# Performance work log

Hardware: AMD Instinct MI355X
Metric: run time of the kernel (lower is better)

Reference implementation:

```python
import jax, jax.numpy as jnp
import numpy as np

B, MAXR = 2048, 512
REQ_IN, REQ_HID, EMB1, EMB2 = 64, 256, 256, 128
INST_IN, CONCAT_HID = 64, 512


def setup_inputs() -> dict:
    key = jax.random.key(0)
    ks = jax.random.split(key, 10)
    inp = {
        "x_inst": jax.random.normal(ks[0], (B, INST_IN), dtype=jnp.float32),
        "x_req": jax.random.normal(ks[1], (B, MAXR, REQ_IN), dtype=jnp.float32),
        "x_n_req": jax.random.randint(ks[2], (B,), 0, MAXR, dtype=jnp.int32),
        # weights stored [in, out]; torch Linear has no bias for the req MLP
        "W_in": jax.random.normal(ks[3], (REQ_IN, REQ_HID), dtype=jnp.float32) / np.sqrt(REQ_IN),
        "W_e1": jax.random.normal(ks[4], (REQ_HID, EMB1), dtype=jnp.float32) / np.sqrt(REQ_HID),
        "W_e2": jax.random.normal(ks[5], (EMB1, EMB2), dtype=jnp.float32) / np.sqrt(EMB1),
        "W_c": jax.random.normal(ks[6], (INST_IN + EMB2, CONCAT_HID), dtype=jnp.float32) / np.sqrt(INST_IN + EMB2),
        "b_c": jax.random.normal(ks[7], (CONCAT_HID,), dtype=jnp.float32) * 0.01,
        "W_o": jax.random.normal(ks[8], (CONCAT_HID, 1), dtype=jnp.float32) / np.sqrt(CONCAT_HID),
        "b_o": jax.random.normal(ks[9], (1,), dtype=jnp.float32) * 0.01,
    }
    return inp


def reference(x_inst, x_req, x_n_req, W_in, W_e1, W_e2, W_c, b_c, W_o, b_o):
    act = jax.nn.relu
    # per-request MLP: [B, MAXR, REQ_IN] -> [B, MAXR, EMB1]
    h = act(jnp.einsum('bri,ih->brh', x_req, W_in))
    h = act(jnp.einsum('brh,he->bre', h, W_e1))
    # mask out padded requests (ragged lengths), then sum-pool over requests
    mask = (jnp.arange(MAXR)[None, :] < x_n_req[:, None])  # [B, MAXR]
    pooled = jnp.einsum('bre,br->be', h, mask.astype(h.dtype))  # [B, EMB1]
    req_embed = act(pooled @ W_e2)  # [B, EMB2]
    x = jnp.concatenate([x_inst, req_embed], axis=1)
    x = act(x @ W_c + b_c)
    return x @ W_o + b_o  # [B, 1]
```

## Files before the change

kernel.cpp:

```cpp
#include <hip/hip_runtime.h>


typedef __bf16 bf16x8 __attribute__((ext_vector_type(8)));
typedef __bf16 bf16x4 __attribute__((ext_vector_type(4)));
typedef float f32x4 __attribute__((ext_vector_type(4)));

#define MFMA16(a, b, c) __builtin_amdgcn_mfma_f32_16x16x32_bf16((a), (b), (c), 0, 0, 0)

#define G_BLOCKS 512

#define ASYNC_COPY16_NT(gsrc, ldst)                                   \
  __builtin_amdgcn_global_load_lds(                                   \
      (__attribute__((address_space(1))) void*)(gsrc),                \
      (__attribute__((address_space(3))) void*)(ldst), 16, 0, 2)

__global__ __launch_bounds__(256) void prep(const float* __restrict__ Win,
                                            const float* __restrict__ We1,
                                            const int* __restrict__ n_req,
                                            __bf16* __restrict__ WinT,
                                            __bf16* __restrict__ We1T,
                                            unsigned int* __restrict__ worklist,
                                            int* __restrict__ wl_count,
                                            float* __restrict__ zbuf) {
  if (blockIdx.x < 320) {
    int t = blockIdx.x * 256 + threadIdx.x;
    if (t < 16384) {
      int nn = t >> 6, k = t & 63;
      WinT[t] = (__bf16)Win[k * 256 + nn];
    } else {
      int e = t - 16384;
      int nn = e >> 8, k = e & 255;
      We1T[e] = (__bf16)We1[k * 256 + nn];
    }
    return;
  }
  ((float4*)zbuf)[threadIdx.x] = make_float4(0.f, 0.f, 0.f, 0.f);
  __shared__ int wsum[4];
  const int tid = threadIdx.x;
  const int base = tid * 8;
  int nt[8], s = 0;
#pragma unroll
  for (int j = 0; j < 8; ++j) {
    int n = n_req[base + j];
    nt[j] = (n + 63) >> 6;
    s += nt[j];
  }
  const int lane = tid & 63, wv = tid >> 6;
  int inc = s;
#pragma unroll
  for (int d = 1; d < 64; d <<= 1) {
    int u = __shfl_up(inc, d);
    if (lane >= d) inc += u;
  }
  if (lane == 63) wsum[wv] = inc;
  __syncthreads();
  int woff = 0;
  for (int w = 0; w < wv; ++w) woff += wsum[w];
  int off = woff + inc - s;
#pragma unroll
  for (int j = 0; j < 8; ++j) {
    int b = base + j;
    for (int t = 0; t < nt[j]; ++t) worklist[off++] = (unsigned int)(b * 8 + t);
  }
  if (tid == 255) wl_count[0] = woff + inc;
}

__global__ __launch_bounds__(512, 4) void mlp_pool(const float* __restrict__ x_req,
                                                   const int* __restrict__ n_req,
                                                   const __bf16* __restrict__ WinT,
                                                   const __bf16* __restrict__ We1T,
                                                   const unsigned int* __restrict__ worklist,
                                                   const int* __restrict__ wl_count,
                                                   const float* __restrict__ zbuf,
                                                   float* __restrict__ part) {
  __shared__ __align__(16) float Af[64 * 64];
  __shared__ __align__(16) __bf16 H[64][264];

  const int tid = threadIdx.x;
  const int wv = tid >> 6;
  const int lane = tid & 63;
  const int llo = lane & 15;
  const int lhi = lane >> 4;
  const int c0 = wv * 32;

  const int count = wl_count[0];
  int i = blockIdx.x;
  if (i >= count) return;

  bf16x8 bw1[2][2];
#pragma unroll
  for (int nf = 0; nf < 2; ++nf)
#pragma unroll
    for (int kk = 0; kk < 2; ++kk)
      bw1[nf][kk] = *(const bf16x8*)(WinT + (c0 + nf * 16 + llo) * 64 +
                                     kk * 32 + lhi * 8);

  unsigned int cit = worklist[i];
  {
    int cb = (int)(cit >> 3), ct = (int)(cit & 7);
    int cv = min(64, n_req[cb] - ct * 64);
    const float* src = x_req + ((size_t)cb * 512 + (size_t)ct * 64) * 64;
#pragma unroll
    for (int s = 0; s < 2; ++s) {
      const int row = wv * 8 + s * 4 + lhi;
      const int gc = llo ^ (row & 15);
      const float* g = (row < cv) ? (src + row * 64 + gc * 4) : (zbuf + llo * 4);
      ASYNC_COPY16_NT(g, Af + (wv * 8 + s * 4) * 64);
    }
  }

  for (; i < count; i += G_BLOCKS) {
    __syncthreads();

    f32x4 acc[4][2];
#pragma unroll
    for (int mi = 0; mi < 4; ++mi)
#pragma unroll
      for (int nf = 0; nf < 2; ++nf) acc[mi][nf] = (f32x4){0.f, 0.f, 0.f, 0.f};
#pragma unroll
    for (int kk = 0; kk < 2; ++kk)
#pragma unroll
      for (int mi = 0; mi < 4; ++mi) {
        const int row = mi * 16 + llo;
        const int cb = kk * 8 + lhi * 2;
        f32x4 lo = *(const f32x4*)(Af + row * 64 + ((cb) ^ llo) * 4);
        f32x4 hi = *(const f32x4*)(Af + row * 64 + ((cb + 1) ^ llo) * 4);
        bf16x8 a;
        a[0] = (__bf16)lo[0]; a[1] = (__bf16)lo[1];
        a[2] = (__bf16)lo[2]; a[3] = (__bf16)lo[3];
        a[4] = (__bf16)hi[0]; a[5] = (__bf16)hi[1];
        a[6] = (__bf16)hi[2]; a[7] = (__bf16)hi[3];
#pragma unroll
        for (int nf = 0; nf < 2; ++nf)
          acc[mi][nf] = MFMA16(bw1[nf][kk], a, acc[mi][nf]);
      }
#pragma unroll
    for (int mi = 0; mi < 4; ++mi)
#pragma unroll
      for (int nf = 0; nf < 2; ++nf) {
        bf16x4 hv;
#pragma unroll
        for (int r = 0; r < 4; ++r) hv[r] = (__bf16)fmaxf(acc[mi][nf][r], 0.f);
        *(bf16x4*)&H[mi * 16 + llo][c0 + nf * 16 + lhi * 4] = hv;
      }
    __syncthreads();

    const int inext = i + G_BLOCKS;
    const bool hn = inext < count;
    unsigned int nit = 0u;
    if (hn) {
      nit = worklist[inext];
      int nb = (int)(nit >> 3), ntl = (int)(nit & 7);
      int nv = min(64, n_req[nb] - ntl * 64);
      const float* nsrc = x_req + ((size_t)nb * 512 + (size_t)ntl * 64) * 64;
#pragma unroll
      for (int s = 0; s < 2; ++s) {
        const int row = wv * 8 + s * 4 + lhi;
        const int gc = llo ^ (row & 15);
        const float* g = (row < nv) ? (nsrc + row * 64 + gc * 4) : (zbuf + llo * 4);
        ASYNC_COPY16_NT(g, Af + (wv * 8 + s * 4) * 64);
      }
    }

#pragma unroll
    for (int mi = 0; mi < 4; ++mi)
#pragma unroll
      for (int nf = 0; nf < 2; ++nf) acc[mi][nf] = (f32x4){0.f, 0.f, 0.f, 0.f};
#pragma unroll
    for (int kk = 0; kk < 8; ++kk) {
      bf16x8 a2[4];
#pragma unroll
      for (int mi = 0; mi < 4; ++mi)
        a2[mi] = *(const bf16x8*)&H[mi * 16 + llo][kk * 32 + lhi * 8];
#pragma unroll
      for (int nf = 0; nf < 2; ++nf) {
        bf16x8 bf_ = *(const bf16x8*)(We1T +
                        (size_t)(c0 + nf * 16 + llo) * 256 +
                        kk * 32 + lhi * 8);
#pragma unroll
        for (int mi = 0; mi < 4; ++mi)
          acc[mi][nf] = MFMA16(a2[mi], bf_, acc[mi][nf]);
      }
    }
    float colsum[2] = {0.f, 0.f};
#pragma unroll
    for (int mi = 0; mi < 4; ++mi)
#pragma unroll
      for (int nf = 0; nf < 2; ++nf)
#pragma unroll
        for (int r = 0; r < 4; ++r)
          colsum[nf] += fmaxf(acc[mi][nf][r], 0.f);

    float* outp = part + (size_t)cit * 256;
#pragma unroll
    for (int nf = 0; nf < 2; ++nf) {
      float s = colsum[nf];
      s += __shfl_xor(s, 16);
      s += __shfl_xor(s, 32);
      if (lane < 16) outp[c0 + nf * 16 + lane] = s;
    }

    cit = nit;
  }
}

__global__ __launch_bounds__(256) void head_kernel(const float* __restrict__ x_inst,
                                                   const float* __restrict__ part,
                                                   const int* __restrict__ n_req,
                                                   const float* __restrict__ We2,
                                                   const float* __restrict__ Wc,
                                                   const float* __restrict__ bc,
                                                   const float* __restrict__ Wo,
                                                   const float* __restrict__ bo,
                                                   float* __restrict__ out) {
  __shared__ float P[16][256];
  __shared__ float XC[16][192];
  __shared__ float RED[4][16];
  const int tid = threadIdx.x;
  const int r0 = blockIdx.x * 16;

#pragma unroll
  for (int i = 0; i < 4; ++i) {
    int flat = tid + i * 256;
    int row = flat >> 6, c4 = flat & 63;
    int ntiles = (n_req[r0 + row] + 63) >> 6;
    float4 s = make_float4(0.f, 0.f, 0.f, 0.f);
    for (int tt = 0; tt < ntiles; ++tt) {
      float4 p = ((const float4*)(part + ((size_t)(r0 + row) * 8 + tt) * 256))[c4];
      s.x += p.x; s.y += p.y; s.z += p.z; s.w += p.w;
    }
    *(float4*)&P[row][c4 * 4] = s;
  }
  {
    int row = tid >> 4, c4 = tid & 15;
    float4 w = ((const float4*)(x_inst + (size_t)(r0 + row) * 64))[c4];
    *(float4*)&XC[row][c4 * 4] = w;
  }
  __syncthreads();

  {
    const int rh = tid >> 7, j = tid & 127;
    float acc[8] = {0.f, 0.f, 0.f, 0.f, 0.f, 0.f, 0.f, 0.f};
    for (int k4 = 0; k4 < 64; ++k4) {
      float w0 = We2[(k4 * 4 + 0) * 128 + j];
      float w1 = We2[(k4 * 4 + 1) * 128 + j];
      float w2 = We2[(k4 * 4 + 2) * 128 + j];
      float w3 = We2[(k4 * 4 + 3) * 128 + j];
#pragma unroll
      for (int rr = 0; rr < 8; ++rr) {
        float4 pv = *(const float4*)&P[rh * 8 + rr][k4 * 4];
        acc[rr] += pv.x * w0 + pv.y * w1 + pv.z * w2 + pv.w * w3;
      }
    }
#pragma unroll
    for (int rr = 0; rr < 8; ++rr)
      XC[rh * 8 + rr][64 + j] = fmaxf(acc[rr], 0.f);
  }
  __syncthreads();

  float part_r[16];
#pragma unroll
  for (int r = 0; r < 16; ++r) part_r[r] = 0.f;
#pragma unroll
  for (int jj = 0; jj < 2; ++jj) {
    const int j = tid + jj * 256;
    float acc[16];
#pragma unroll
    for (int r = 0; r < 16; ++r) acc[r] = 0.f;
    for (int k4 = 0; k4 < 48; ++k4) {
      float w0 = Wc[(k4 * 4 + 0) * 512 + j];
      float w1 = Wc[(k4 * 4 + 1) * 512 + j];
      float w2 = Wc[(k4 * 4 + 2) * 512 + j];
      float w3 = Wc[(k4 * 4 + 3) * 512 + j];
#pragma unroll
      for (int r = 0; r < 16; ++r) {
        float4 xv = *(const float4*)&XC[r][k4 * 4];
        acc[r] += xv.x * w0 + xv.y * w1 + xv.z * w2 + xv.w * w3;
      }
    }
    const float bcv = bc[j], wov = Wo[j];
#pragma unroll
    for (int r = 0; r < 16; ++r)
      part_r[r] += fmaxf(acc[r] + bcv, 0.f) * wov;
  }
#pragma unroll
  for (int r = 0; r < 16; ++r) {
    part_r[r] += __shfl_xor(part_r[r], 1);
    part_r[r] += __shfl_xor(part_r[r], 2);
    part_r[r] += __shfl_xor(part_r[r], 4);
    part_r[r] += __shfl_xor(part_r[r], 8);
    part_r[r] += __shfl_xor(part_r[r], 16);
    part_r[r] += __shfl_xor(part_r[r], 32);
  }
  const int wvv = tid >> 6, lane = tid & 63;
  if (lane == 0) {
#pragma unroll
    for (int r = 0; r < 16; ++r) RED[wvv][r] = part_r[r];
  }
  __syncthreads();
  if (tid < 16)
    out[r0 + tid] = RED[0][tid] + RED[1][tid] + RED[2][tid] + RED[3][tid] + bo[0];
}

extern "C" void kernel_launch(void* const* d_in, const int* in_sizes, int n_in,
                              void* d_out, int out_size, void* d_ws, size_t ws_size,
                              hipStream_t stream) {
  const float* x_inst = (const float*)d_in[0];
  const float* x_req  = (const float*)d_in[1];
  const int*   n_req  = (const int*)d_in[2];
  const float* W_in   = (const float*)d_in[3];
  const float* W_e1   = (const float*)d_in[4];
  const float* W_e2   = (const float*)d_in[5];
  const float* W_c    = (const float*)d_in[6];
  const float* b_c    = (const float*)d_in[7];
  const float* W_o    = (const float*)d_in[8];
  const float* b_o    = (const float*)d_in[9];
  float* out = (float*)d_out;

  char* ws = (char*)d_ws;
  const size_t PART_BYTES = (size_t)2048 * 8 * 256 * 4;
  float*        partbuf  = (float*)ws;
  __bf16*       WinT     = (__bf16*)(ws + PART_BYTES);
  __bf16*       We1T     = (__bf16*)(ws + PART_BYTES + (32 << 10));
  unsigned int* worklist = (unsigned int*)(ws + PART_BYTES + (160 << 10));
  int*          wl_count = (int*)(ws + PART_BYTES + (224 << 10));
  float*        zbuf     = (float*)(ws + PART_BYTES + (228 << 10));

  prep<<<321, 256, 0, stream>>>(W_in, W_e1, n_req, WinT, We1T, worklist,
                                wl_count, zbuf);
  mlp_pool<<<G_BLOCKS, 512, 0, stream>>>(x_req, n_req, WinT, We1T, worklist,
                                         wl_count, zbuf, partbuf);
  head_kernel<<<128, 256, 0, stream>>>(x_inst, partbuf, n_req, W_e2, W_c, b_c,
                                       W_o, b_o, out);
}
```

Before: 218.7 us.

## Pre-convert A tile to bf16 in LDS, coalesce prep, shrink head rows per block

Three separate changes. The prep transpose now reads the weights coalesced and scatters the writes. mlp_pool converts the fp32 input tile to bf16 once into a padded LDS buffer, so the MFMA loop does single 16-byte loads instead of converting twice per wave (each of the 8 waves was reconverting the same tile). This adds a barrier per iteration. The head kernel processes 4 rows per block instead of 16 and launches 512 blocks for more parallelism, but weights are re-read by 4x more blocks.

```diff
diff --git a/kernel.cpp b/kernel.cpp
--- a/kernel.cpp
+++ b/kernel.cpp
@@ -25,12 +25,12 @@
   if (blockIdx.x < 320) {
     int t = blockIdx.x * 256 + threadIdx.x;
     if (t < 16384) {
-      int nn = t >> 6, k = t & 63;
-      WinT[t] = (__bf16)Win[k * 256 + nn];
+      int k = t >> 8, nn = t & 255;
+      WinT[nn * 64 + k] = (__bf16)Win[t];
     } else {
       int e = t - 16384;
-      int nn = e >> 8, k = e & 255;
-      We1T[e] = (__bf16)We1[k * 256 + nn];
+      int k = e >> 8, nn = e & 255;
+      We1T[nn * 256 + k] = (__bf16)We1[e];
     }
     return;
   }
@@ -74,6 +74,7 @@
                                                    const float* __restrict__ zbuf,
                                                    float* __restrict__ part) {
   __shared__ __align__(16) float Af[64 * 64];
+  __shared__ __align__(16) __bf16 Ab[64][72];
   __shared__ __align__(16) __bf16 H[64][264];
 
   const int tid = threadIdx.x;
@@ -112,28 +113,40 @@
   for (; i < count; i += G_BLOCKS) {
     __syncthreads();
 
+    {
+      const int crow = wv * 8 + (lane >> 3);
+      const int cc = lane & 7;
+      const int r15 = crow & 15;
+      f32x4 r0 = *(const f32x4*)(Af + crow * 64 + (cc ^ r15) * 4);
+      f32x4 r1 = *(const f32x4*)(Af + crow * 64 + ((cc | 8) ^ r15) * 4);
+      bf16x4 w0, w1;
+#pragma unroll
+      for (int j = 0; j < 4; ++j) {
+        w0[j] = (__bf16)r0[j];
+        w1[j] = (__bf16)r1[j];
+      }
+      *(bf16x4*)&Ab[crow][cc * 4] = w0;
+      *(bf16x4*)&Ab[crow][32 + cc * 4] = w1;
+    }
+    __syncthreads();
+
     f32x4 acc[4][2];
 #pragma unroll
     for (int mi = 0; mi < 4; ++mi)
 #pragma unroll
       for (int nf = 0; nf < 2; ++nf) acc[mi][nf] = (f32x4){0.f, 0.f, 0.f, 0.f};
 #pragma unroll
-    for (int kk = 0; kk < 2; ++kk)
-#pragma unroll
-      for (int mi = 0; mi < 4; ++mi) {
-        const int row = mi * 16 + llo;
-        const int cb = kk * 8 + lhi * 2;
-        f32x4 lo = *(const f32x4*)(Af + row * 64 + ((cb) ^ llo) * 4);
-        f32x4 hi = *(const f32x4*)(Af + row * 64 + ((cb + 1) ^ llo) * 4);
-        bf16x8 a;
-        a[0] = (__bf16)lo[0]; a[1] = (__bf16)lo[1];
-        a[2] = (__bf16)lo[2]; a[3] = (__bf16)lo[3];
-        a[4] = (__bf16)hi[0]; a[5] = (__bf16)hi[1];
-        a[6] = (__bf16)hi[2]; a[7] = (__bf16)hi[3];
+    for (int kk = 0; kk < 2; ++kk) {
+      bf16x8 af[4];
+#pragma unroll
+      for (int mi = 0; mi < 4; ++mi)
+        af[mi] = *(const bf16x8*)&Ab[mi * 16 + llo][kk * 32 + lhi * 8];
+#pragma unroll
+      for (int mi = 0; mi < 4; ++mi)
 #pragma unroll
         for (int nf = 0; nf < 2; ++nf)
-          acc[mi][nf] = MFMA16(bw1[nf][kk], a, acc[mi][nf]);
-      }
+          acc[mi][nf] = MFMA16(bw1[nf][kk], af[mi], acc[mi][nf]);
+    }
 #pragma unroll
     for (int mi = 0; mi < 4; ++mi)
 #pragma unroll
@@ -213,16 +226,14 @@
                                                    const float* __restrict__ Wo,
                                                    const float* __restrict__ bo,
                                                    float* __restrict__ out) {
-  __shared__ float P[16][256];
-  __shared__ float XC[16][192];
-  __shared__ float RED[4][16];
+  __shared__ float P[4][256];
+  __shared__ float XC[4][192];
+  __shared__ float RED[4][4];
   const int tid = threadIdx.x;
-  const int r0 = blockIdx.x * 16;
-
-#pragma unroll
-  for (int i = 0; i < 4; ++i) {
-    int flat = tid + i * 256;
-    int row = flat >> 6, c4 = flat & 63;
+  const int r0 = blockIdx.x * 4;
+
+  {
+    int row = tid >> 6, c4 = tid & 63;
     int ntiles = (n_req[r0 + row] + 63) >> 6;
     float4 s = make_float4(0.f, 0.f, 0.f, 0.f);
     for (int tt = 0; tt < ntiles; ++tt) {
@@ -231,7 +242,7 @@
     }
     *(float4*)&P[row][c4 * 4] = s;
   }
-  {
+  if (tid < 64) {
     int row = tid >> 4, c4 = tid & 15;
     float4 w = ((const float4*)(x_inst + (size_t)(r0 + row) * 64))[c4];
     *(float4*)&XC[row][c4 * 4] = w;
@@ -240,65 +251,61 @@
 
   {
     const int rh = tid >> 7, j = tid & 127;
-    float acc[8] = {0.f, 0.f, 0.f, 0.f, 0.f, 0.f, 0.f, 0.f};
+    float acc[2] = {0.f, 0.f};
     for (int k4 = 0; k4 < 64; ++k4) {
       float w0 = We2[(k4 * 4 + 0) * 128 + j];
       float w1 = We2[(k4 * 4 + 1) * 128 + j];
       float w2 = We2[(k4 * 4 + 2) * 128 + j];
       float w3 = We2[(k4 * 4 + 3) * 128 + j];
 #pragma unroll
-      for (int rr = 0; rr < 8; ++rr) {
-        float4 pv = *(const float4*)&P[rh * 8 + rr][k4 * 4];
+      for (int rr = 0; rr < 2; ++rr) {
+        float4 pv = *(const float4*)&P[rh * 2 + rr][k4 * 4];
         acc[rr] += pv.x * w0 + pv.y * w1 + pv.z * w2 + pv.w * w3;
       }
     }
 #pragma unroll
-    for (int rr = 0; rr < 8; ++rr)
-      XC[rh * 8 + rr][64 + j] = fmaxf(acc[rr], 0.f);
+    for (int rr = 0; rr < 2; ++rr)
+      XC[rh * 2 + rr][64 + j] = fmaxf(acc[rr], 0.f);
   }
   __syncthreads();
 
-  float part_r[16];
-#pragma unroll
-  for (int r = 0; r < 16; ++r) part_r[r] = 0.f;
+  float pr[4] = {0.f, 0.f, 0.f, 0.f};
 #pragma unroll
   for (int jj = 0; jj < 2; ++jj) {
     const int j = tid + jj * 256;
-    float acc[16];
-#pragma unroll
-    for (int r = 0; r < 16; ++r) acc[r] = 0.f;
+    float acc[4] = {0.f, 0.f, 0.f, 0.f};
     for (int k4 = 0; k4 < 48; ++k4) {
       float w0 = Wc[(k4 * 4 + 0) * 512 + j];
       float w1 = Wc[(k4 * 4 + 1) * 512 + j];
       float w2 = Wc[(k4 * 4 + 2) * 512 + j];
       float w3 = Wc[(k4 * 4 + 3) * 512 + j];
 #pragma unroll
-      for (int r = 0; r < 16; ++r) {
+      for (int r = 0; r < 4; ++r) {
         float4 xv = *(const float4*)&XC[r][k4 * 4];
         acc[r] += xv.x * w0 + xv.y * w1 + xv.z * w2 + xv.w * w3;
       }
     }
     const float bcv = bc[j], wov = Wo[j];
 #pragma unroll
-    for (int r = 0; r < 16; ++r)
-      part_r[r] += fmaxf(acc[r] + bcv, 0.f) * wov;
-  }
-#pragma unroll
-  for (int r = 0; r < 16; ++r) {
-    part_r[r] += __shfl_xor(part_r[r], 1);
-    part_r[r] += __shfl_xor(part_r[r], 2);
-    part_r[r] += __shfl_xor(part_r[r], 4);
-    part_r[r] += __shfl_xor(part_r[r], 8);
-    part_r[r] += __shfl_xor(part_r[r], 16);
-    part_r[r] += __shfl_xor(part_r[r], 32);
+    for (int r = 0; r < 4; ++r)
+      pr[r] += fmaxf(acc[r] + bcv, 0.f) * wov;
+  }
+#pragma unroll
+  for (int r = 0; r < 4; ++r) {
+    pr[r] += __shfl_xor(pr[r], 1);
+    pr[r] += __shfl_xor(pr[r], 2);
+    pr[r] += __shfl_xor(pr[r], 4);
+    pr[r] += __shfl_xor(pr[r], 8);
+    pr[r] += __shfl_xor(pr[r], 16);
+    pr[r] += __shfl_xor(pr[r], 32);
   }
   const int wvv = tid >> 6, lane = tid & 63;
   if (lane == 0) {
 #pragma unroll
-    for (int r = 0; r < 16; ++r) RED[wvv][r] = part_r[r];
+    for (int r = 0; r < 4; ++r) RED[wvv][r] = pr[r];
   }
   __syncthreads();
-  if (tid < 16)
+  if (tid < 4)
     out[r0 + tid] = RED[0][tid] + RED[1][tid] + RED[2][tid] + RED[3][tid] + bo[0];
 }
 
@@ -330,6 +337,6 @@
                                 wl_count, zbuf);
   mlp_pool<<<G_BLOCKS, 512, 0, stream>>>(x_req, n_req, WinT, We1T, worklist,
                                          wl_count, zbuf, partbuf);
-  head_kernel<<<128, 256, 0, stream>>>(x_inst, partbuf, n_req, W_e2, W_c, b_c,
+  head_kernel<<<512, 256, 0, stream>>>(x_inst, partbuf, n_req, W_e2, W_c, b_c,
                                        W_o, b_o, out);
 }
```

Result: faster. 198.9 us (-9.1%).
